# Kernel tuning notes

Hardware: AMD Instinct MI355X
Metric: run time of the kernel (lower is better)

Reference implementation:

```python
import jax, jax.numpy as jnp
import numpy as np

B, N, D, H = 4, 1024, 768, 12
HD = D // H
HID = 4 * D
EPS = 1e-5


def setup_inputs():
    key = jax.random.key(0)
    ks = iter(jax.random.split(key, 64))
    def rnd(*shape):
        return jax.random.normal(next(ks), shape, jnp.float32) * 0.02
    d = {
        "img_tok": jax.random.normal(next(ks), (B, N, D), jnp.float32),
        "evt_tok": jax.random.normal(next(ks), (B, N, D), jnp.float32),
    }
    for nm in ["ln_q1", "ln_kv1", "ln_q2", "ln_kv2", "ln_mi", "ln_me"]:
        d[nm + "_g"] = jnp.ones((D,), jnp.float32)
        d[nm + "_b"] = jnp.zeros((D,), jnp.float32)
    for p in ["si", "se"]:
        d[p + "_qkv_w"] = rnd(D, 3 * D)
        d[p + "_qkv_b"] = jnp.zeros((3 * D,), jnp.float32)
        d[p + "_proj_w"] = rnd(D, D)
        d[p + "_proj_b"] = jnp.zeros((D,), jnp.float32)
    for p in ["xei", "xie"]:
        for m in ["q", "k", "v", "p"]:
            d[p + "_" + m + "_w"] = rnd(D, D)
            d[p + "_" + m + "_b"] = jnp.zeros((D,), jnp.float32)
    for p in ["mi", "me"]:
        d[p + "_fc1_w"] = rnd(D, HID)
        d[p + "_fc1_b"] = jnp.zeros((HID,), jnp.float32)
        d[p + "_fc2_w"] = rnd(HID, D)
        d[p + "_fc2_b"] = jnp.zeros((D,), jnp.float32)
    return d


def _ln(x, g, b):
    m = jnp.mean(x, -1, keepdims=True)
    v = jnp.mean((x - m) ** 2, -1, keepdims=True)
    return (x - m) * jax.lax.rsqrt(v + EPS) * g + b


def _self_attn(x, qkv_w, qkv_b, p_w, p_b):
    qkv = (x @ qkv_w + qkv_b).reshape(B, N, 3, H, HD)
    q, k, v = qkv[:, :, 0], qkv[:, :, 1], qkv[:, :, 2]  # each (B,N,H,HD)
    s = jnp.einsum("bqhd,bkhd->bhqk", q, k) * (HD ** -0.5)
    a = jax.nn.softmax(s, -1)
    o = jnp.einsum("bhqk,bkhd->bqhd", a, v).reshape(B, N, D)
    return o @ p_w + p_b


def _cross_attn(qx, kvx, q_w, q_b, k_w, k_b, v_w, v_b, p_w, p_b):
    q = (qx @ q_w + q_b).reshape(B, N, H, HD)
    k = (kvx @ k_w + k_b).reshape(B, N, H, HD)
    v = (kvx @ v_w + v_b).reshape(B, N, H, HD)
    # invert_softmax=True: negate scores before softmax
    s = -(jnp.einsum("bqhd,bkhd->bhqk", q, k) * (HD ** -0.5))
    a = jax.nn.softmax(s, -1)
    o = jnp.einsum("bhqk,bkhd->bqhd", a, v).reshape(B, N, D)
    return o @ p_w + p_b


def _mlp(x, w1, b1, w2, b2):
    return jax.nn.gelu(x @ w1 + b1, approximate=False) @ w2 + b2


def _fwd(img_tok, evt_tok,
         ln_q1_g, ln_q1_b, ln_kv1_g, ln_kv1_b,
         si_qkv_w, si_qkv_b, si_proj_w, si_proj_b,
         se_qkv_w, se_qkv_b, se_proj_w, se_proj_b,
         ln_q2_g, ln_q2_b, ln_kv2_g, ln_kv2_b,
         xei_q_w, xei_q_b, xei_k_w, xei_k_b, xei_v_w, xei_v_b, xei_p_w, xei_p_b,
         xie_q_w, xie_q_b, xie_k_w, xie_k_b, xie_v_w, xie_v_b, xie_p_w, xie_p_b,
         ln_mi_g, ln_mi_b, mi_fc1_w, mi_fc1_b, mi_fc2_w, mi_fc2_b,
         ln_me_g, ln_me_b, me_fc1_w, me_fc1_b, me_fc2_w, me_fc2_b):
    img = img_tok + _self_attn(_ln(img_tok, ln_q1_g, ln_q1_b),
                               si_qkv_w, si_qkv_b, si_proj_w, si_proj_b)
    evt = evt_tok + _self_attn(_ln(evt_tok, ln_kv1_g, ln_kv1_b),
                               se_qkv_w, se_qkv_b, se_proj_w, se_proj_b)
    i1, e1 = img, evt
    # shared norm_q2 / norm_kv2 weights across both cross-attn directions
    img = i1 + _cross_attn(_ln(i1, ln_q2_g, ln_q2_b), _ln(e1, ln_kv2_g, ln_kv2_b),
                           xei_q_w, xei_q_b, xei_k_w, xei_k_b, xei_v_w, xei_v_b,
                           xei_p_w, xei_p_b)
    evt = e1 + _cross_attn(_ln(e1, ln_q2_g, ln_q2_b), _ln(i1, ln_kv2_g, ln_kv2_b),
                           xie_q_w, xie_q_b, xie_k_w, xie_k_b, xie_v_w, xie_v_b,
                           xie_p_w, xie_p_b)
    img = img + _mlp(_ln(img, ln_mi_g, ln_mi_b), mi_fc1_w, mi_fc1_b, mi_fc2_w, mi_fc2_b)
    evt = evt + _mlp(_ln(evt, ln_me_g, ln_me_b), me_fc1_w, me_fc1_b, me_fc2_w, me_fc2_b)
    return img, evt


def reference(img_tok, evt_tok,
              ln_q1_g, ln_q1_b, ln_kv1_g, ln_kv1_b,
              si_qkv_w, si_qkv_b, si_proj_w, si_proj_b,
              se_qkv_w, se_qkv_b, se_proj_w, se_proj_b,
              ln_q2_g, ln_q2_b, ln_kv2_g, ln_kv2_b,
              xei_q_w, xei_q_b, xei_k_w, xei_k_b, xei_v_w, xei_v_b, xei_p_w, xei_p_b,
              xie_q_w, xie_q_b, xie_k_w, xie_k_b, xie_v_w, xie_v_b, xie_p_w, xie_p_b,
              ln_mi_g, ln_mi_b, mi_fc1_w, mi_fc1_b, mi_fc2_w, mi_fc2_b,
              ln_me_g, ln_me_b, me_fc1_w, me_fc1_b, me_fc2_w, me_fc2_b):
    return _fwd(img_tok, evt_tok,
                ln_q1_g, ln_q1_b, ln_kv1_g, ln_kv1_b,
                si_qkv_w, si_qkv_b, si_proj_w, si_proj_b,
                se_qkv_w, se_qkv_b, se_proj_w, se_proj_b,
                ln_q2_g, ln_q2_b, ln_kv2_g, ln_kv2_b,
                xei_q_w, xei_q_b, xei_k_w, xei_k_b, xei_v_w, xei_v_b, xei_p_w, xei_p_b,
                xie_q_w, xie_q_b, xie_k_w, xie_k_b, xie_v_w, xie_v_b, xie_p_w, xie_p_b,
                ln_mi_g, ln_mi_b, mi_fc1_w, mi_fc1_b, mi_fc2_w, mi_fc2_b,
                ln_me_g, ln_me_b, me_fc1_w, me_fc1_b, me_fc2_w, me_fc2_b)
```

## Files before the change

kernel.cpp:

```cpp
#include <hip/hip_runtime.h>

constexpr int cB  = 4;
constexpr int cN  = 1024;
constexpr int cD  = 768;
constexpr int cH  = 12;
constexpr int cHD = 64;
constexpr int cHID = 3072;
constexpr int cBN = cB * cN;

typedef __attribute__((ext_vector_type(8))) short bf16x8;
typedef __attribute__((ext_vector_type(4))) float f32x4;

static __device__ __forceinline__ unsigned short f2bf(float f) {
    union { float f; unsigned int u; } v; v.f = f;
    unsigned int u = v.u;
    return (unsigned short)((u + 0x7FFFu + ((u >> 16) & 1u)) >> 16);
}

static __device__ __forceinline__ void gl_lds16(const void* g, void* l) {
    __builtin_amdgcn_global_load_lds(
        (const __attribute__((address_space(1))) unsigned int*)g,
        (__attribute__((address_space(3))) unsigned int*)l, 16, 0, 0);
}

struct WcTab {
    const float* src[16];
    unsigned long long dstoff[16];
    int K[16];
    int N[16];
    int start[17];
};

__global__ __launch_bounds__(256)
void wconv_all(WcTab tab, unsigned short* __restrict__ WoBase) {
    int b = blockIdx.x;
    int i = 0;
    while (i < 15 && b >= tab.start[i + 1]) i++;
    const float* __restrict__ W = tab.src[i];
    unsigned short* __restrict__ Wo = WoBase + tab.dstoff[i];
    int K = tab.K[i], N = tab.N[i];
    int tb = b - tab.start[i];
    int Kt = K >> 6;
    int k0 = (tb % Kt) * 64, n0 = (tb / Kt) * 64;

    __shared__ float Ls[64][68];
    int t = threadIdx.x;
    int lr = t >> 4, lc = (t & 15) * 4;
    #pragma unroll
    for (int q = 0; q < 4; q++) {
        float4 v = *(const float4*)&W[(size_t)(k0 + lr + q * 16) * N + n0 + lc];
        Ls[lr + q * 16][lc + 0] = v.x;  Ls[lr + q * 16][lc + 1] = v.y;
        Ls[lr + q * 16][lc + 2] = v.z;  Ls[lr + q * 16][lc + 3] = v.w;
    }
    __syncthreads();
    int mt = t >> 3;
    int nb = mt & 3, kb = mt >> 2;
    int sub = t & 7;
    int K8 = K >> 3;
    size_t chunk = ((size_t)(n0 / 16 + nb) * K8 + (size_t)(k0 / 8 + kb)) * 128;
    unsigned short buf[16];
    #pragma unroll
    for (int rr = 0; rr < 2; rr++) {
        int n_r = sub * 2 + rr;
        #pragma unroll
        for (int kk = 0; kk < 8; kk++)
            buf[rr * 8 + kk] = f2bf(Ls[kb * 8 + kk][nb * 16 + n_r]);
    }
    uint4 w0, w1;
    w0.x = buf[0] | ((unsigned)buf[1] << 16);   w0.y = buf[2] | ((unsigned)buf[3] << 16);
    w0.z = buf[4] | ((unsigned)buf[5] << 16);   w0.w = buf[6] | ((unsigned)buf[7] << 16);
    w1.x = buf[8] | ((unsigned)buf[9] << 16);   w1.y = buf[10] | ((unsigned)buf[11] << 16);
    w1.z = buf[12] | ((unsigned)buf[13] << 16); w1.w = buf[14] | ((unsigned)buf[15] << 16);
    *(uint4*)&Wo[chunk + sub * 16]     = w0;
    *(uint4*)&Wo[chunk + sub * 16 + 8] = w1;
}

static __device__ __forceinline__ void ln_body(const float* __restrict__ x,
                                               const float* __restrict__ g,
                                               const float* __restrict__ b,
                                               unsigned short* __restrict__ y,
                                               int R) {
    __shared__ float psum[16][17], psq[16][17];
    __shared__ float mean_s[16], rstd_s[16];
    int t = threadIdx.x;
    int r = t >> 4, c16 = t & 15;
    const float* xr = x + ((size_t)R * 16 + r) * cD;
    float s = 0.f, sq = 0.f;
    #pragma unroll
    for (int i = 0; i < 12; i++) {
        float4 v = *(const float4*)&xr[c16 * 4 + i * 64];
        s  += v.x + v.y + v.z + v.w;
        sq += v.x * v.x + v.y * v.y + v.z * v.z + v.w * v.w;
    }
    psum[r][c16] = s; psq[r][c16] = sq;
    __syncthreads();
    if (t < 16) {
        float ss = 0.f, qq = 0.f;
        #pragma unroll
        for (int i = 0; i < 16; i++) { ss += psum[t][i]; qq += psq[t][i]; }
        float m = ss / (float)cD;
        mean_s[t] = m;
        rstd_s[t] = rsqrtf(qq / (float)cD - m * m + 1e-5f);
    }
    __syncthreads();
    int r2 = t & 15, cslot = t >> 4;
    const float* xr2 = x + ((size_t)R * 16 + r2) * cD;
    float m = mean_s[r2], rs = rstd_s[r2];
    for (int c = cslot; c < 96; c += 16) {
        float4 a0 = *(const float4*)&xr2[c * 8];
        float4 a1 = *(const float4*)&xr2[c * 8 + 4];
        float4 g0 = *(const float4*)&g[c * 8];
        float4 g1 = *(const float4*)&g[c * 8 + 4];
        float4 b0 = *(const float4*)&b[c * 8];
        float4 b1 = *(const float4*)&b[c * 8 + 4];
        unsigned short o[8];
        o[0] = f2bf((a0.x - m) * rs * g0.x + b0.x);
        o[1] = f2bf((a0.y - m) * rs * g0.y + b0.y);
        o[2] = f2bf((a0.z - m) * rs * g0.z + b0.z);
        o[3] = f2bf((a0.w - m) * rs * g0.w + b0.w);
        o[4] = f2bf((a1.x - m) * rs * g1.x + b1.x);
        o[5] = f2bf((a1.y - m) * rs * g1.y + b1.y);
        o[6] = f2bf((a1.z - m) * rs * g1.z + b1.z);
        o[7] = f2bf((a1.w - m) * rs * g1.w + b1.w);
        uint4 w;
        w.x = o[0] | ((unsigned)o[1] << 16); w.y = o[2] | ((unsigned)o[3] << 16);
        w.z = o[4] | ((unsigned)o[5] << 16); w.w = o[6] | ((unsigned)o[7] << 16);
        *(uint4*)&y[((size_t)R * 96 + c) * 128 + r2 * 8] = w;
    }
}

struct LnTab {
    const float* x[4];
    const float* g[4];
    const float* b[4];
    unsigned short* y[4];
};

__global__ __launch_bounds__(256)
void ln4_kernel(LnTab T) {
    int s = blockIdx.x >> 8;
    ln_body(T.x[s], T.g[s], T.b[s], T.y[s], blockIdx.x & 255);
}

struct GPair {
    const unsigned short* A0;  const unsigned short* A1;
    const unsigned short* B0;  const unsigned short* B1;
    const float* bias0;        const float* bias1;
    const float* biasB0;       const float* biasB1;
    const float* res0;         const float* res1;
    void* C0;                  void* C1;
    unsigned short* V0;        unsigned short* V1;
};

template<int NBUF>
__global__ __launch_bounds__(256, 4)
void mfma_gemm(GPair P, int K, int N, int ostride, int vsplit, int mode) {
    __shared__ bf16x8 aT[NBUF][512];
    __shared__ bf16x8 bT[NBUF][256];
    constexpr int AH = NBUF - 1;
    int z = blockIdx.z;
    const unsigned short* A   = z ? P.A1 : P.A0;
    const unsigned short* Bw  = z ? P.B1 : P.B0;
    const float* bias  = z ? P.bias1  : P.bias0;
    const float* biasB = z ? P.biasB1 : P.biasB0;
    const float* res   = z ? P.res1   : P.res0;
    void* Cout         = z ? P.C1     : P.C0;
    unsigned short* VtOut = z ? P.V1  : P.V0;

    int t = threadIdx.x;
    int w = t >> 6, l = t & 63;
    int m0 = blockIdx.x * 128, n0 = blockIdx.y * 64;
    int K8 = K >> 3;

    f32x4 acc[2][4];
    #pragma unroll
    for (int i = 0; i < 2; i++)
        #pragma unroll
        for (int j = 0; j < 4; j++) acc[i][j] = (f32x4){0.f, 0.f, 0.f, 0.f};

    int sA0 = w * 128 + l;
    int sA1 = sA0 + 64;
    int sB  = w * 64 + l;
    int ciA0 = sA0 >> 4, ciA1 = sA1 >> 4, ciB = sB >> 4;
    const unsigned short* pA0 = A +
        ((size_t)((m0 >> 4) + (ciA0 >> 2)) * K8 + (ciA0 & 3)) * 128 + (sA0 & 15) * 8;
    const unsigned short* pA1 = A +
        ((size_t)((m0 >> 4) + (ciA1 >> 2)) * K8 + (ciA1 & 3)) * 128 + (sA1 & 15) * 8;
    const unsigned short* pB  = Bw +
        ((size_t)((n0 >> 4) + (ciB >> 2)) * K8 + (ciB & 3)) * 128 + (sB & 15) * 8;

    auto stage = [&](int buf, int step) {
        size_t off = (size_t)step * 512;
        gl_lds16(pA0 + off, &aT[buf][w * 128]);
        gl_lds16(pA1 + off, &aT[buf][w * 128 + 64]);
        gl_lds16(pB  + off, &bT[buf][w * 64]);
    };

    int nsteps = K >> 5;
    #pragma unroll
    for (int p = 0; p < AH; p++) stage(p, p);
    for (int s = 0; s < nsteps; s++) {
        int cb = s % NBUF;
        int rem = nsteps - 1 - s;
        if (s + AH < nsteps) {
            stage((s + AH) % NBUF, s + AH);
            if constexpr (NBUF == 4) asm volatile("s_waitcnt vmcnt(9)" ::: "memory");
            else                     asm volatile("s_waitcnt vmcnt(6)" ::: "memory");
        } else if (rem == 2) {
            asm volatile("s_waitcnt vmcnt(6)" ::: "memory");
        } else if (rem == 1) {
            asm volatile("s_waitcnt vmcnt(3)" ::: "memory");
        } else {
            asm volatile("s_waitcnt vmcnt(0)" ::: "memory");
        }
        __builtin_amdgcn_s_barrier();

        bf16x8 av[2], bv[4];
        #pragma unroll
        for (int i = 0; i < 2; i++) av[i] = aT[cb][(2 * w + i) * 64 + l];
        #pragma unroll
        for (int j = 0; j < 4; j++) bv[j] = bT[cb][j * 64 + l];
        #pragma unroll
        for (int i = 0; i < 2; i++)
            #pragma unroll
            for (int j = 0; j < 4; j++)
                acc[i][j] = __builtin_amdgcn_mfma_f32_16x16x32_bf16(av[i], bv[j], acc[i][j], 0, 0, 0);

        asm volatile("s_waitcnt lgkmcnt(0)" ::: "memory");
        __builtin_amdgcn_s_barrier();
    }

    int col = l & 15;
    int rb = (l >> 4) * 4;
    int mw = m0 + w * 32;
    if (mode == 2) {
        float* out = (float*)Cout;
        #pragma unroll
        for (int j = 0; j < 4; j++) {
            int n = n0 + j * 16 + col;
            float bj = bias[n];
            #pragma unroll
            for (int i = 0; i < 2; i++)
                #pragma unroll
                for (int r = 0; r < 4; r++) {
                    int mm = mw + i * 16 + rb + r;
                    out[(size_t)mm * ostride + n] = acc[i][j][r] + bj + res[(size_t)mm * ostride + n];
                }
        }
    } else if (mode == 1) {
        unsigned short* out = (unsigned short*)Cout;
        int N8 = N >> 3;
        #pragma unroll
        for (int j = 0; j < 4; j++) {
            int n = n0 + j * 16 + col;
            float bj = bias[n];
            #pragma unroll
            for (int i = 0; i < 2; i++)
                #pragma unroll
                for (int r = 0; r < 4; r++) {
                    int mm = mw + i * 16 + rb + r;
                    float v = acc[i][j][r] + bj;
                    v = 0.5f * v * (1.0f + erff(v * 0.70710678118f));
                    size_t ad = ((size_t)(mm >> 4) * N8 + (n >> 3)) * 128 + (mm & 15) * 8 + (n & 7);
                    out[ad] = f2bf(v);
                }
        }
    } else {
        bool toVt = (mode == 3) && (n0 >= vsplit);
        if (!toVt) {
            unsigned short* out = (unsigned short*)Cout;
            #pragma unroll
            for (int j = 0; j < 4; j++) {
                int n = n0 + j * 16 + col;
                float bj = bias[n];
                #pragma unroll
                for (int i = 0; i < 2; i++)
                    #pragma unroll
                    for (int r = 0; r < 4; r++) {
                        int mm = mw + i * 16 + rb + r;
                        out[(size_t)mm * ostride + n] = f2bf(acc[i][j][r] + bj);
                    }
            }
        } else {
            #pragma unroll
            for (int j = 0; j < 4; j++) {
                int n = n0 + j * 16 + col;
                int vc = n - vsplit;
                float bj = biasB[vc];
                int ph = vc >> 6, d = vc & 63;
                #pragma unroll
                for (int i = 0; i < 2; i++) {
                    int mm = mw + i * 16 + rb;
                    int bbv = mm >> 10, tok = mm & 1023;
                    unsigned short q0 = f2bf(acc[i][j][0] + bj);
                    unsigned short q1 = f2bf(acc[i][j][1] + bj);
                    unsigned short q2 = f2bf(acc[i][j][2] + bj);
                    unsigned short q3 = f2bf(acc[i][j][3] + bj);
                    uint2 pk;
                    pk.x = q0 | ((unsigned)q1 << 16);
                    pk.y = q2 | ((unsigned)q3 << 16);
                    size_t ad = ((size_t)(bbv * 12 + ph) * 64 + d) * 1024 + tok;
                    *(uint2*)&VtOut[ad] = pk;
                }
            }
        }
    }
}

__global__ __launch_bounds__(256, 2)
void fattn_kernel(const unsigned short* __restrict__ Q0,
                  const unsigned short* __restrict__ Q1,
                  const unsigned short* __restrict__ Kq0,
                  const unsigned short* __restrict__ Kq1,
                  const unsigned short* __restrict__ Vt0,
                  const unsigned short* __restrict__ Vt1,
                  unsigned short* __restrict__ Oo0,
                  unsigned short* __restrict__ Oo1,
                  int qk_stride, float scale) {
    __shared__ unsigned short Kls[2][4096];
    __shared__ unsigned short Vls[2][4096];
    __shared__ unsigned short Ps[4][16][72];

    int z = blockIdx.z;
    const unsigned short* Qp = z ? Q1 : Q0;
    const unsigned short* Kp = z ? Kq1 : Kq0;
    const unsigned short* Vt = z ? Vt1 : Vt0;
    unsigned short* O        = z ? Oo1 : Oo0;

    int t = threadIdx.x;
    int w = t >> 6, l = t & 63;
    int la = l & 15, lb = l >> 4;
    int swz = la & 7;
    int blk = blockIdx.x;
    int qt0 = (blk & 15) * 64 + w * 16;
    int bh = blk >> 4;
    int h = bh % cH, bb = bh / cH;

    const unsigned short* Qb = Qp + (size_t)(bb * cN) * qk_stride + h * cHD;
    const unsigned short* Kb = Kp + (size_t)(bb * cN) * qk_stride + h * cHD;
    const unsigned short* Vb = Vt + (size_t)(bb * cH + h) * (64 * 1024);

    bf16x8 av[2];
    #pragma unroll
    for (int s = 0; s < 2; s++)
        av[s] = *(const bf16x8*)(Qb + (size_t)(qt0 + la) * qk_stride + 32 * s + 8 * lb);

    int ch0 = w * 128 + l;
    int ch1 = ch0 + 64;
    int r0 = ch0 >> 3, c0 = (ch0 & 7) ^ (r0 & 7);
    int r1 = ch1 >> 3, c1 = (ch1 & 7) ^ (r1 & 7);
    const unsigned short* K0 = Kb + (size_t)r0 * qk_stride + c0 * 8;
    const unsigned short* K1 = Kb + (size_t)r1 * qk_stride + c1 * 8;
    const unsigned short* V0 = Vb + (size_t)r0 * 1024 + c0 * 8;
    const unsigned short* V1 = Vb + (size_t)r1 * 1024 + c1 * 8;
    int dst0 = w * 1024;
    int dst1 = dst0 + 512;

    auto stage = [&](int buf, int kt0) {
        gl_lds16(K0 + (size_t)kt0 * qk_stride, &Kls[buf][dst0]);
        gl_lds16(K1 + (size_t)kt0 * qk_stride, &Kls[buf][dst1]);
        gl_lds16(V0 + kt0, &Vls[buf][dst0]);
        gl_lds16(V1 + kt0, &Vls[buf][dst1]);
    };

    float m_run[4], l_run[4];
    f32x4 acc_o[4];
    #pragma unroll
    for (int r = 0; r < 4; r++) { m_run[r] = -1e30f; l_run[r] = 0.f; }
    #pragma unroll
    for (int nt = 0; nt < 4; nt++) acc_o[nt] = (f32x4){0.f, 0.f, 0.f, 0.f};

    stage(0, 0);
    for (int it = 0; it < 16; it++) {
        int cb = it & 1;
        if (it < 15) {
            stage(cb ^ 1, (it + 1) << 6);
            asm volatile("s_waitcnt vmcnt(4)" ::: "memory");
        } else {
            asm volatile("s_waitcnt vmcnt(0)" ::: "memory");
        }
        __builtin_amdgcn_s_barrier();
        asm volatile("" ::: "memory");

        bf16x8 kf[4][2];
        #pragma unroll
        for (int j = 0; j < 4; j++)
            #pragma unroll
            for (int s = 0; s < 2; s++)
                kf[j][s] = *(const bf16x8*)&Kls[cb][(16 * j + la) * 64 + (((4 * s + lb) ^ swz) << 3)];

        f32x4 sj[4];
        #pragma unroll
        for (int j = 0; j < 4; j++) sj[j] = (f32x4){0.f, 0.f, 0.f, 0.f};
        #pragma unroll
        for (int j = 0; j < 4; j++)
            #pragma unroll
            for (int s = 0; s < 2; s++)
                sj[j] = __builtin_amdgcn_mfma_f32_16x16x32_bf16(av[s], kf[j][s], sj[j], 0, 0, 0);

        float x[4][4];
        #pragma unroll
        for (int j = 0; j < 4; j++)
            #pragma unroll
            for (int r = 0; r < 4; r++) x[j][r] = sj[j][r] * scale;
        float mt[4];
        #pragma unroll
        for (int r = 0; r < 4; r++)
            mt[r] = fmaxf(fmaxf(x[0][r], x[1][r]), fmaxf(x[2][r], x[3][r]));
        #pragma unroll
        for (int off = 1; off <= 8; off <<= 1)
            #pragma unroll
            for (int r = 0; r < 4; r++)
                mt[r] = fmaxf(mt[r], __shfl_xor(mt[r], off, 64));
        float al[4];
        #pragma unroll
        for (int r = 0; r < 4; r++) {
            float mn = fmaxf(m_run[r], mt[r]);
            al[r] = __expf(m_run[r] - mn);
            m_run[r] = mn;
        }
        float p[4][4], ts[4] = {0.f, 0.f, 0.f, 0.f};
        #pragma unroll
        for (int j = 0; j < 4; j++)
            #pragma unroll
            for (int r = 0; r < 4; r++) {
                p[j][r] = __expf(x[j][r] - m_run[r]);
                ts[r] += p[j][r];
            }
        #pragma unroll
        for (int off = 1; off <= 8; off <<= 1)
            #pragma unroll
            for (int r = 0; r < 4; r++)
                ts[r] += __shfl_xor(ts[r], off, 64);
        #pragma unroll
        for (int r = 0; r < 4; r++) l_run[r] = l_run[r] * al[r] + ts[r];
        #pragma unroll
        for (int nt = 0; nt < 4; nt++)
            #pragma unroll
            for (int r = 0; r < 4; r++) acc_o[nt][r] *= al[r];

        #pragma unroll
        for (int j = 0; j < 4; j++)
            #pragma unroll
            for (int r = 0; r < 4; r++)
                Ps[w][lb * 4 + r][16 * j + la] = f2bf(p[j][r]);
        asm volatile("s_waitcnt lgkmcnt(0)" ::: "memory");
        bf16x8 pf[2];
        #pragma unroll
        for (int s = 0; s < 2; s++)
            pf[s] = *(const bf16x8*)&Ps[w][la][32 * s + 8 * lb];

        bf16x8 vf[4][2];
        #pragma unroll
        for (int nt = 0; nt < 4; nt++)
            #pragma unroll
            for (int s = 0; s < 2; s++)
                vf[nt][s] = *(const bf16x8*)&Vls[cb][(16 * nt + la) * 64 + (((4 * s + lb) ^ swz) << 3)];
        #pragma unroll
        for (int nt = 0; nt < 4; nt++)
            #pragma unroll
            for (int s = 0; s < 2; s++)
                acc_o[nt] = __builtin_amdgcn_mfma_f32_16x16x32_bf16(pf[s], vf[nt][s], acc_o[nt], 0, 0, 0);

        asm volatile("s_waitcnt lgkmcnt(0)" ::: "memory");
        __builtin_amdgcn_s_barrier();
    }

    float inv[4];
    #pragma unroll
    for (int r = 0; r < 4; r++) inv[r] = 1.0f / l_run[r];
    size_t mhi = ((size_t)bb * cN + qt0) >> 4;
    #pragma unroll
    for (int nt = 0; nt < 4; nt++) {
        int k = h * cHD + 16 * nt + la;
        size_t base = (mhi * 96 + (k >> 3)) * 128 + (k & 7);
        #pragma unroll
        for (int r = 0; r < 4; r++) {
            unsigned short val = f2bf(acc_o[nt][r] * inv[r]);
            O[base + (lb * 4 + r) * 8] = val;
        }
    }
}

extern "C" void kernel_launch(void* const* d_in, const int* in_sizes, int n_in,
                              void* d_out, int out_size, void* d_ws, size_t ws_size,
                              hipStream_t stream) {
    const float* img_tok  = (const float*)d_in[0];
    const float* evt_tok  = (const float*)d_in[1];
    const float* ln_q1_g  = (const float*)d_in[2];
    const float* ln_q1_b  = (const float*)d_in[3];
    const float* ln_kv1_g = (const float*)d_in[4];
    const float* ln_kv1_b = (const float*)d_in[5];
    const float* ln_q2_g  = (const float*)d_in[6];
    const float* ln_q2_b  = (const float*)d_in[7];
    const float* ln_kv2_g = (const float*)d_in[8];
    const float* ln_kv2_b = (const float*)d_in[9];
    const float* ln_mi_g  = (const float*)d_in[10];
    const float* ln_mi_b  = (const float*)d_in[11];
    const float* ln_me_g  = (const float*)d_in[12];
    const float* ln_me_b  = (const float*)d_in[13];
    const float* si_qkv_w  = (const float*)d_in[14];
    const float* si_qkv_b  = (const float*)d_in[15];
    const float* si_proj_w = (const float*)d_in[16];
    const float* si_proj_b = (const float*)d_in[17];
    const float* se_qkv_w  = (const float*)d_in[18];
    const float* se_qkv_b  = (const float*)d_in[19];
    const float* se_proj_w = (const float*)d_in[20];
    const float* se_proj_b = (const float*)d_in[21];
    const float* xei_q_w = (const float*)d_in[22];
    const float* xei_q_b = (const float*)d_in[23];
    const float* xei_k_w = (const float*)d_in[24];
    const float* xei_k_b = (const float*)d_in[25];
    const float* xei_v_w = (const float*)d_in[26];
    const float* xei_v_b = (const float*)d_in[27];
    const float* xei_p_w = (const float*)d_in[28];
    const float* xei_p_b = (const float*)d_in[29];
    const float* xie_q_w = (const float*)d_in[30];
    const float* xie_q_b = (const float*)d_in[31];
    const float* xie_k_w = (const float*)d_in[32];
    const float* xie_k_b = (const float*)d_in[33];
    const float* xie_v_w = (const float*)d_in[34];
    const float* xie_v_b = (const float*)d_in[35];
    const float* xie_p_w = (const float*)d_in[36];
    const float* xie_p_b = (const float*)d_in[37];
    const float* mi_fc1_w = (const float*)d_in[38];
    const float* mi_fc1_b = (const float*)d_in[39];
    const float* mi_fc2_w = (const float*)d_in[40];
    const float* mi_fc2_b = (const float*)d_in[41];
    const float* me_fc1_w = (const float*)d_in[42];
    const float* me_fc1_b = (const float*)d_in[43];
    const float* me_fc2_w = (const float*)d_in[44];
    const float* me_fc2_b = (const float*)d_in[45];

    const size_t U = (size_t)cBN * cD;
    unsigned short* wsb = (unsigned short*)d_ws;
    unsigned short* Wz  = wsb;
    unsigned short* LNo = wsb + 18874368;
    unsigned short* AO  = LNo + U;
    unsigned short* T1  = AO + U;
    unsigned short* Vt  = T1 + 3 * U;
    unsigned short* T1b  = Vt + U;
    unsigned short* Vtb  = T1b + 3 * U;
    unsigned short* Hidb = Vtb + U;
    float* out_img = (float*)d_out;
    float* out_evt = out_img + U;

    const bool big = ws_size >= (size_t)(18874368 + 14 * U) * 2;

    const size_t O_SI_QKV = 0,        O_SE_QKV = 1769472;
    const size_t O_SI_P   = 3538944,  O_SE_P   = 4128768;
    const size_t O_XEI_Q  = 4718592,  O_XEI_KV = 5308416, O_XEI_P = 6488064;
    const size_t O_XIE_Q  = 7077888,  O_XIE_KV = 7667712, O_XIE_P = 8847360;
    const size_t O_MI_F1  = 9437184,  O_MI_F2  = 11796480;
    const size_t O_ME_F1  = 14155776, O_ME_F2  = 16515072;

    {
        WcTab tab;
        const float* srcs[16] = { si_qkv_w, se_qkv_w, si_proj_w, se_proj_w,
                                  xei_q_w, xei_k_w, xei_v_w, xei_p_w,
                                  xie_q_w, xie_k_w, xie_v_w, xie_p_w,
                                  mi_fc1_w, mi_fc2_w, me_fc1_w, me_fc2_w };
        const size_t offs[16] = { O_SI_QKV, O_SE_QKV, O_SI_P, O_SE_P,
                                  O_XEI_Q, O_XEI_KV, O_XEI_KV + 589824, O_XEI_P,
                                  O_XIE_Q, O_XIE_KV, O_XIE_KV + 589824, O_XIE_P,
                                  O_MI_F1, O_MI_F2, O_ME_F1, O_ME_F2 };
        const int Ks[16] = { 768, 768, 768, 768, 768, 768, 768, 768,
                             768, 768, 768, 768, 768, 3072, 768, 3072 };
        const int Ns[16] = { 2304, 2304, 768, 768, 768, 768, 768, 768,
                             768, 768, 768, 768, 3072, 768, 3072, 768 };
        int acc = 0;
        for (int i = 0; i < 16; i++) {
            tab.src[i] = srcs[i];
            tab.dstoff[i] = offs[i];
            tab.K[i] = Ks[i];
            tab.N[i] = Ns[i];
            tab.start[i] = acc;
            acc += (Ks[i] / 64) * (Ns[i] / 64);
        }
        tab.start[16] = acc;
        hipLaunchKernelGGL(wconv_all, dim3(acc), dim3(256), 0, stream, tab, Wz);
    }

    const float SC = 0.125f;

    auto lnN = [&](int nsets, const float* x0, const float* g0, const float* b0, unsigned short* y0,
                   const float* x1, const float* g1, const float* b1, unsigned short* y1,
                   const float* x2, const float* g2, const float* b2, unsigned short* y2,
                   const float* x3, const float* g3, const float* b3, unsigned short* y3) {
        LnTab T = {{x0, x1, x2, x3}, {g0, g1, g2, g3}, {b0, b1, b2, b3}, {y0, y1, y2, y3}};
        hipLaunchKernelGGL(ln4_kernel, dim3(nsets * 256), dim3(256), 0, stream, T);
    };
    auto gemm2 = [&](dim3 grid, GPair P, int K_, int N_, int ostride_, int vsplit_, int mode_) {
        int blocks = grid.x * grid.y * grid.z;
        if (blocks <= 768)
            hipLaunchKernelGGL(mfma_gemm<4>, grid, dim3(256), 0, stream, P, K_, N_, ostride_, vsplit_, mode_);
        else
            hipLaunchKernelGGL(mfma_gemm<3>, grid, dim3(256), 0, stream, P, K_, N_, ostride_, vsplit_, mode_);
    };
    auto attn2 = [&](int nz, const unsigned short* q0, const unsigned short* k0, const unsigned short* v0, unsigned short* o0,
                     const unsigned short* q1, const unsigned short* k1, const unsigned short* v1, unsigned short* o1,
                     float sc) {
        hipLaunchKernelGGL(fattn_kernel, dim3(cB * cH * 16, 1, nz), dim3(256), 0, stream,
                           q0, q1, k0, k1, v0, v1, o0, o1, 2304, sc);
    };

    if (big) {
        lnN(2, img_tok, ln_q1_g, ln_q1_b, LNo,  evt_tok, ln_kv1_g, ln_kv1_b, AO,
               img_tok, ln_q1_g, ln_q1_b, LNo,  img_tok, ln_q1_g, ln_q1_b, LNo);
        gemm2(dim3(32, 36, 2),
              {LNo, AO, Wz + O_SI_QKV, Wz + O_SE_QKV, si_qkv_b, se_qkv_b,
               si_qkv_b + 1536, se_qkv_b + 1536, nullptr, nullptr, T1, T1b, Vt, Vtb},
              768, 2304, 2304, 1536, 3);
        attn2(2, T1, T1 + 768, Vt, LNo,  T1b, T1b + 768, Vtb, AO, SC);
        gemm2(dim3(32, 12, 2),
              {LNo, AO, Wz + O_SI_P, Wz + O_SE_P, si_proj_b, se_proj_b,
               nullptr, nullptr, img_tok, evt_tok, out_img, out_evt, nullptr, nullptr},
              768, 768, 768, 0, 2);
        lnN(4, out_img, ln_q2_g, ln_q2_b, LNo,   out_evt, ln_kv2_g, ln_kv2_b, AO,
               out_img, ln_kv2_g, ln_kv2_b, Hidb, out_evt, ln_q2_g, ln_q2_b, Hidb + U);
        gemm2(dim3(32, 12, 2),
              {LNo, Hidb + U, Wz + O_XEI_Q, Wz + O_XIE_Q, xei_q_b, xie_q_b,
               nullptr, nullptr, nullptr, nullptr, T1, T1b, nullptr, nullptr},
              768, 768, 2304, 1 << 30, 0);
        gemm2(dim3(32, 24, 2),
              {AO, Hidb, Wz + O_XEI_KV, Wz + O_XIE_KV, xei_k_b, xie_k_b,
               xei_v_b, xie_v_b, nullptr, nullptr, T1 + 768, T1b + 768, Vt, Vtb},
              768, 1536, 2304, 768, 3);
        attn2(2, T1, T1 + 768, Vt, LNo,  T1b, T1b + 768, Vtb, AO, -SC);
        gemm2(dim3(32, 12, 2),
              {LNo, AO, Wz + O_XEI_P, Wz + O_XIE_P, xei_p_b, xie_p_b,
               nullptr, nullptr, out_img, out_evt, out_img, out_evt, nullptr, nullptr},
              768, 768, 768, 0, 2);
        lnN(2, out_img, ln_mi_g, ln_mi_b, LNo,  out_evt, ln_me_g, ln_me_b, AO,
               out_img, ln_mi_g, ln_mi_b, LNo,  out_img, ln_mi_g, ln_mi_b, LNo);
        gemm2(dim3(32, 48, 2),
              {LNo, AO, Wz + O_MI_F1, Wz + O_ME_F1, mi_fc1_b, me_fc1_b,
               nullptr, nullptr, nullptr, nullptr, T1, Hidb, nullptr, nullptr},
              768, 3072, 3072, 0, 1);
        gemm2(dim3(32, 12, 2),
              {T1, Hidb, Wz + O_MI_F2, Wz + O_ME_F2, mi_fc2_b, me_fc2_b,
               nullptr, nullptr, out_img, out_evt, out_img, out_evt, nullptr, nullptr},
              3072, 768, 768, 0, 2);
    } else {
        unsigned short* Hid = AO;
        auto ln1 = [&](const float* x_, const float* g_, const float* b_, unsigned short* y_) {
            lnN(1, x_, g_, b_, y_, x_, g_, b_, y_, x_, g_, b_, y_, x_, g_, b_, y_);
        };
        auto gemm1 = [&](const unsigned short* A_, size_t woff, const float* b_, const float* bB_,
                         const float* r_, void* C_, unsigned short* V_, int K_, int N_,
                         int ostride_, int vsplit_, int mode_) {
            gemm2(dim3(cBN / 128, N_ / 64, 1),
                  {A_, A_, Wz + woff, Wz + woff, b_, b_, bB_, bB_, r_, r_, C_, C_, V_, V_},
                  K_, N_, ostride_, vsplit_, mode_);
        };
        auto attn1 = [&](const unsigned short* q_, const unsigned short* k_,
                         unsigned short* o_, float sc_) {
            attn2(1, q_, k_, Vt, o_, q_, k_, Vt, o_, sc_);
        };

        ln1(img_tok, ln_q1_g, ln_q1_b, LNo);
        gemm1(LNo, O_SI_QKV, si_qkv_b, si_qkv_b + 1536, nullptr, T1, Vt, 768, 2304, 2304, 1536, 3);
        attn1(T1, T1 + 768, AO, SC);
        gemm1(AO, O_SI_P, si_proj_b, nullptr, img_tok, out_img, Vt, 768, 768, 768, 0, 2);

        ln1(evt_tok, ln_kv1_g, ln_kv1_b, LNo);
        gemm1(LNo, O_SE_QKV, se_qkv_b, se_qkv_b + 1536, nullptr, T1, Vt, 768, 2304, 2304, 1536, 3);
        attn1(T1, T1 + 768, AO, SC);
        gemm1(AO, O_SE_P, se_proj_b, nullptr, evt_tok, out_evt, Vt, 768, 768, 768, 0, 2);

        ln1(out_img, ln_q2_g, ln_q2_b, LNo);
        gemm1(LNo, O_XEI_Q, xei_q_b, nullptr, nullptr, T1, Vt, 768, 768, 2304, 1 << 30, 0);
        ln1(out_evt, ln_kv2_g, ln_kv2_b, LNo);
        gemm1(LNo, O_XEI_KV, xei_k_b, xei_v_b, nullptr, T1 + 768, Vt, 768, 1536, 2304, 768, 3);
        attn1(T1, T1 + 768, AO, -SC);

        ln1(out_img, ln_kv2_g, ln_kv2_b, LNo);
        gemm1(LNo, O_XIE_KV, xie_k_b, xie_v_b, nullptr, T1 + 768, Vt, 768, 1536, 2304, 768, 3);
        ln1(out_evt, ln_q2_g, ln_q2_b, LNo);
        gemm1(LNo, O_XIE_Q, xie_q_b, nullptr, nullptr, T1, Vt, 768, 768, 2304, 1 << 30, 0);

        gemm1(AO, O_XEI_P, xei_p_b, nullptr, out_img, out_img, Vt, 768, 768, 768, 0, 2);
        attn1(T1, T1 + 768, AO, -SC);
        gemm1(AO, O_XIE_P, xie_p_b, nullptr, out_evt, out_evt, Vt, 768, 768, 768, 0, 2);

        lnN(2, out_img, ln_mi_g, ln_mi_b, LNo,  out_evt, ln_me_g, ln_me_b, Vt,
               out_img, ln_mi_g, ln_mi_b, LNo,  out_img, ln_mi_g, ln_mi_b, LNo);
        gemm1(LNo, O_MI_F1, mi_fc1_b, nullptr, nullptr, Hid, Vt, 768, 3072, 3072, 0, 1);
        gemm1(Hid, O_MI_F2, mi_fc2_b, nullptr, out_img, out_img, Vt, 3072, 768, 768, 0, 2);
        gemm1(Vt,  O_ME_F1, me_fc1_b, nullptr, nullptr, Hid, Vt, 768, 3072, 3072, 0, 1);
        gemm1(Hid, O_ME_F2, me_fc2_b, nullptr, out_evt, out_evt, Vt, 3072, 768, 768, 0, 2);
    }
}
```

Measured before the change: 698.2 us.

## Restructure flash-attention softmax with exp2, lazy rescale, and MFMA row sums

The attention inner loop now folds log2(e) into the score scale and uses exp2. The running max is only raised when a tile's max exceeds it by more than a threshold, checked wave-uniformly, which skips most rescaling of the accumulators. The softmax row sum comes from an extra MFMA against a ones vector instead of shuffle reductions, and probabilities are packed to bf16 with a hardware pack-convert instruction. This trades two extra MFMAs per tile and an occasional recomputation of exp for fewer VALU and cross-lane operations. Exponentials can grow up to 2^11 before rescaling, which may affect precision slightly.

```diff
diff --git a/kernel.cpp b/kernel.cpp
--- a/kernel.cpp
+++ b/kernel.cpp
@@ -363,10 +363,16 @@
         gl_lds16(V1 + kt0, &Vls[buf][dst1]);
     };
 
-    float m_run[4], l_run[4];
-    f32x4 acc_o[4];
-    #pragma unroll
-    for (int r = 0; r < 4; r++) { m_run[r] = -1e30f; l_run[r] = 0.f; }
+    const float sc2 = scale * 1.44269504f;
+    bf16x8 ones;
+    #pragma unroll
+    for (int e = 0; e < 8; e++) ones[e] = (short)0x3F80;
+
+    float m2[4];
+    f32x4 acc_o[4], acc_l;
+    #pragma unroll
+    for (int r = 0; r < 4; r++) m2[r] = -1e30f;
+    acc_l = (f32x4){0.f, 0.f, 0.f, 0.f};
     #pragma unroll
     for (int nt = 0; nt < 4; nt++) acc_o[nt] = (f32x4){0.f, 0.f, 0.f, 0.f};
 
@@ -398,52 +404,58 @@
             for (int s = 0; s < 2; s++)
                 sj[j] = __builtin_amdgcn_mfma_f32_16x16x32_bf16(av[s], kf[j][s], sj[j], 0, 0, 0);
 
-        float x[4][4];
+        float x2[4][4];
         #pragma unroll
         for (int j = 0; j < 4; j++)
             #pragma unroll
-            for (int r = 0; r < 4; r++) x[j][r] = sj[j][r] * scale;
-        float mt[4];
+            for (int r = 0; r < 4; r++) x2[j][r] = sj[j][r] * sc2;
+
+        float p[4][4];
+        #pragma unroll
+        for (int j = 0; j < 4; j++)
+            #pragma unroll
+            for (int r = 0; r < 4; r++)
+                p[j][r] = __builtin_amdgcn_exp2f(x2[j][r] - m2[r]);
+
+        float mt2[4];
         #pragma unroll
         for (int r = 0; r < 4; r++)
-            mt[r] = fmaxf(fmaxf(x[0][r], x[1][r]), fmaxf(x[2][r], x[3][r]));
+            mt2[r] = fmaxf(fmaxf(x2[0][r], x2[1][r]), fmaxf(x2[2][r], x2[3][r]));
         #pragma unroll
         for (int off = 1; off <= 8; off <<= 1)
             #pragma unroll
             for (int r = 0; r < 4; r++)
-                mt[r] = fmaxf(mt[r], __shfl_xor(mt[r], off, 64));
-        float al[4];
-        #pragma unroll
-        for (int r = 0; r < 4; r++) {
-            float mn = fmaxf(m_run[r], mt[r]);
-            al[r] = __expf(m_run[r] - mn);
-            m_run[r] = mn;
+                mt2[r] = fmaxf(mt2[r], __shfl_xor(mt2[r], off, 64));
+
+        int ok = (mt2[0] <= m2[0] + 11.f) && (mt2[1] <= m2[1] + 11.f) &&
+                 (mt2[2] <= m2[2] + 11.f) && (mt2[3] <= m2[3] + 11.f);
+        if (!__all(ok)) {
+            #pragma unroll
+            for (int r = 0; r < 4; r++) {
+                float mn = fmaxf(m2[r], mt2[r]);
+                float al = __builtin_amdgcn_exp2f(m2[r] - mn);
+                acc_l[r] *= al;
+                #pragma unroll
+                for (int nt = 0; nt < 4; nt++) acc_o[nt][r] *= al;
+                m2[r] = mn;
+            }
+            #pragma unroll
+            for (int j = 0; j < 4; j++)
+                #pragma unroll
+                for (int r = 0; r < 4; r++)
+                    p[j][r] = __builtin_amdgcn_exp2f(x2[j][r] - m2[r]);
         }
-        float p[4][4], ts[4] = {0.f, 0.f, 0.f, 0.f};
+
         #pragma unroll
         for (int j = 0; j < 4; j++)
             #pragma unroll
-            for (int r = 0; r < 4; r++) {
-                p[j][r] = __expf(x[j][r] - m_run[r]);
-                ts[r] += p[j][r];
+            for (int rp = 0; rp < 2; rp++) {
+                unsigned u;
+                asm("v_cvt_pk_bf16_f32 %0, %1, %2"
+                    : "=v"(u) : "v"(p[j][2 * rp]), "v"(p[j][2 * rp + 1]));
+                Ps[w][lb * 4 + 2 * rp][16 * j + la]     = (unsigned short)u;
+                Ps[w][lb * 4 + 2 * rp + 1][16 * j + la] = (unsigned short)(u >> 16);
             }
-        #pragma unroll
-        for (int off = 1; off <= 8; off <<= 1)
-            #pragma unroll
-            for (int r = 0; r < 4; r++)
-                ts[r] += __shfl_xor(ts[r], off, 64);
-        #pragma unroll
-        for (int r = 0; r < 4; r++) l_run[r] = l_run[r] * al[r] + ts[r];
-        #pragma unroll
-        for (int nt = 0; nt < 4; nt++)
-            #pragma unroll
-            for (int r = 0; r < 4; r++) acc_o[nt][r] *= al[r];
-
-        #pragma unroll
-        for (int j = 0; j < 4; j++)
-            #pragma unroll
-            for (int r = 0; r < 4; r++)
-                Ps[w][lb * 4 + r][16 * j + la] = f2bf(p[j][r]);
         asm volatile("s_waitcnt lgkmcnt(0)" ::: "memory");
         bf16x8 pf[2];
         #pragma unroll
@@ -461,6 +473,9 @@
             #pragma unroll
             for (int s = 0; s < 2; s++)
                 acc_o[nt] = __builtin_amdgcn_mfma_f32_16x16x32_bf16(pf[s], vf[nt][s], acc_o[nt], 0, 0, 0);
+        #pragma unroll
+        for (int s = 0; s < 2; s++)
+            acc_l = __builtin_amdgcn_mfma_f32_16x16x32_bf16(pf[s], ones, acc_l, 0, 0, 0);
 
         asm volatile("s_waitcnt lgkmcnt(0)" ::: "memory");
         __builtin_amdgcn_s_barrier();
@@ -468,7 +483,7 @@
 
     float inv[4];
     #pragma unroll
-    for (int r = 0; r < 4; r++) inv[r] = 1.0f / l_run[r];
+    for (int r = 0; r < 4; r++) inv[r] = 1.0f / acc_l[r];
     size_t mhi = ((size_t)bb * cN + qt0) >> 4;
     #pragma unroll
     for (int nt = 0; nt < 4; nt++) {
```

Result: faster. 662.3 us (-5.1%).
